# Performance work log

Measured on AMD Instinct MI355X. Metric: run time of the kernel, lower is better.

The kernel has to match this reference:

```python
import jax, jax.numpy as jnp
import numpy as np

T = 100      # sequence length / output times
B = 2048     # batch
DT = 0.02    # euler step == spacing of ts -> one step per interval
CLAMP = 6.0
LOG2PI = float(np.log(2.0 * np.pi))
sp = jax.nn.softplus


def setup_inputs() -> dict:
    key = jax.random.key(0)
    ks = jax.random.split(key, 20)
    rn = lambda k, s, sc=1.0: jax.random.normal(k, s, dtype=jnp.float32) * sc
    inp = {}
    inp['xs'] = rn(ks[0], (T, B, 3, 50))
    inp['ts'] = jnp.arange(T, dtype=jnp.float32) * DT
    inp['eps0'] = rn(ks[1], (B, 6))
    inp['dW'] = rn(ks[2], (T - 1, B, 6)) * np.sqrt(DT)  # Brownian increments ~ N(0, dt)
    # encoder: 150->30->30->15
    inp['eW1'] = rn(ks[3], (150, 30), 150 ** -0.5); inp['eb1'] = jnp.zeros((30,), jnp.float32)
    inp['eW2'] = rn(ks[4], (30, 30), 30 ** -0.5);   inp['eb2'] = jnp.zeros((30,), jnp.float32)
    inp['eW3'] = rn(ks[5], (30, 15), 30 ** -0.5);   inp['eb3'] = jnp.zeros((15,), jnp.float32)
    # decoder: 6->30->30->100
    inp['dcW1'] = rn(ks[6], (6, 30), 6 ** -0.5);    inp['dcb1'] = jnp.zeros((30,), jnp.float32)
    inp['dcW2'] = rn(ks[7], (30, 30), 30 ** -0.5);  inp['dcb2'] = jnp.zeros((30,), jnp.float32)
    inp['dcW3'] = rn(ks[8], (30, 100), 30 ** -0.5); inp['dcb3'] = jnp.zeros((100,), jnp.float32)
    # f_net: (6+1+3)=10 -> 30 -> 6
    inp['fW1'] = rn(ks[9], (10, 30), 10 ** -0.5);   inp['fb1'] = jnp.zeros((30,), jnp.float32)
    inp['fW2'] = rn(ks[10], (30, 6), 30 ** -0.5);   inp['fb2'] = jnp.zeros((6,), jnp.float32)
    # h_net: (6+1)=7 -> 30 -> 6
    inp['hW1'] = rn(ks[11], (7, 30), 7 ** -0.5);    inp['hb1'] = jnp.zeros((30,), jnp.float32)
    inp['hW2'] = rn(ks[12], (30, 6), 30 ** -0.5);   inp['hb2'] = jnp.zeros((6,), jnp.float32)
    # 6 g_nets stacked: 2 -> 30 -> 1 (sigmoid)
    inp['gW1'] = rn(ks[13], (6, 2, 30), 2 ** -0.5); inp['gb1'] = jnp.zeros((6, 30), jnp.float32)
    inp['gW2'] = rn(ks[14], (6, 30, 1), 30 ** -0.5); inp['gb2'] = jnp.zeros((6, 1), jnp.float32)
    inp['pz0_mean'] = jnp.zeros((1, 6), jnp.float32)
    inp['pz0_logstd'] = jnp.zeros((1, 6), jnp.float32)
    return inp


def _forward(xs, ts, eps0, dW, eW1, eb1, eW2, eb2, eW3, eb3,
             dcW1, dcb1, dcW2, dcb2, dcW3, dcb3,
             fW1, fb1, fW2, fb2, hW1, hb1, hW2, hb2,
             gW1, gb1, gW2, gb2, pz0_mean, pz0_logstd):
    # ---- encoder on time-reversed xs ----
    xse = jnp.flip(xs, 0).reshape(T, B, 150)
    e = sp(xse @ eW1 + eb1)
    e = sp(e @ eW2 + eb2)
    e = e @ eW3 + eb3                         # [T,B,15]
    qz0_mean = e[-1, :, :6]
    qz0_logstd = e[-1, :, 6:12]
    ctx = jnp.flip(e[..., 12:15], 0)           # [T,B,3]

    z0 = qz0_mean + jnp.exp(jnp.clip(qz0_logstd, -CLAMP, CLAMP)) * eps0

    # ---- Euler-Maruyama with logqp (one step per ts interval) ----
    def step(z, sc):
        k, dWk = sc
        t = ts[k]
        dtk = ts[k + 1] - ts[k]
        c = ctx[jnp.minimum(k + 1, T - 1)]     # searchsorted(ts, t, right=True) clamped
        tb = jnp.broadcast_to(t, (B, 1)).astype(z.dtype)
        f = sp(jnp.concatenate([tb, z, c], 1) @ fW1 + fb1) @ fW2 + fb2
        h = sp(jnp.concatenate([tb, z], 1) @ hW1 + hb1) @ hW2 + hb2
        gin = jnp.stack([jnp.broadcast_to(t, (B, 6)).astype(z.dtype), z], -1)  # [B,6,2]
        gh = sp(jnp.einsum('bdi,dih->bdh', gin, gW1) + gb1)
        g = jax.nn.sigmoid(jnp.einsum('bdh,dho->bdo', gh, gW2) + gb2)[..., 0]  # [B,6]
        u = (f - h) / g
        logr = 0.5 * jnp.sum(u * u, axis=1) * dtk   # [B]
        zn = z + f * dtk + g * dWk
        return zn, (zn, logr)

    _, (zs_tail, log_ratio) = jax.lax.scan(step, z0, (jnp.arange(T - 1), dW))
    zs = jnp.concatenate([z0[None], zs_tail], 0)   # [T,B,6]

    # ---- decoder + likelihood ----
    d = sp(zs @ dcW1 + dcb1)
    d = sp(d @ dcW2 + dcb2)
    d = d @ dcW3 + dcb3                        # [T,B,100]
    xm, xl = d[..., :50], d[..., 50:]
    xsig = jnp.exp(jnp.clip(xl, -CLAMP, CLAMP))
    tgt = xs[:, :, -1, :]
    lp = -0.5 * ((tgt - xm) / xsig) ** 2 - jnp.log(xsig) - 0.5 * LOG2PI
    log_pxs = jnp.mean(jnp.sum(lp, axis=(0, 2)))

    # ---- KL(q(z0)||p(z0)) + path term ----
    sq = jnp.exp(jnp.clip(qz0_logstd, -CLAMP, CLAMP))
    spz = jnp.exp(jnp.clip(pz0_logstd, -CLAMP, CLAMP))
    kl = jnp.log(spz / sq) + (sq ** 2 + (qz0_mean - pz0_mean) ** 2) / (2.0 * spz ** 2) - 0.5
    logqp0 = jnp.mean(jnp.sum(kl, axis=1))
    logqp_path = jnp.mean(jnp.sum(log_ratio, axis=0))
    return log_pxs, logqp0 + logqp_path


def reference(xs, ts, eps0, dW, eW1, eb1, eW2, eb2, eW3, eb3,
              dcW1, dcb1, dcW2, dcb2, dcW3, dcb3,
              fW1, fb1, fW2, fb2, hW1, hb1, hW2, hb2,
              gW1, gb1, gW2, gb2, pz0_mean, pz0_logstd):
    return _forward(xs, ts, eps0, dW, eW1, eb1, eW2, eb2, eW3, eb3,
                    dcW1, dcb1, dcW2, dcb2, dcW3, dcb3,
                    fW1, fb1, fW2, fb2, hW1, hb1, hW2, hb2,
                    gW1, gb1, gW2, gb2, pz0_mean, pz0_logstd)
```

## Files before the change

### kernel.cpp

```cpp
#include <hip/hip_runtime.h>
#include <hip/hip_bf16.h>
#include <math.h>

#define Tn 100
#define Bn 2048

typedef int v2i __attribute__((ext_vector_type(2)));
typedef _Float16 h2v __attribute__((ext_vector_type(2)));

__device__ __forceinline__ float sp_f(float x) {
    float e = __expf(-fabsf(x));
    return fmaxf(x, 0.f) + __logf(1.f + e);
}
__device__ __forceinline__ float clamp6(float x) {
    return fminf(fmaxf(x, -6.f), 6.f);
}
__device__ __forceinline__ unsigned int packh2(float a, float b) {
    h2v h; h.x = (_Float16)a; h.y = (_Float16)b;
    return __builtin_bit_cast(unsigned int, h);
}
__device__ __forceinline__ float dot2f(unsigned int a, unsigned int b, float c) {
#if __has_builtin(__builtin_amdgcn_fdot2)
    return __builtin_amdgcn_fdot2(__builtin_bit_cast(h2v, a),
                                  __builtin_bit_cast(h2v, b), c, false);
#else
    h2v ha = __builtin_bit_cast(h2v, a), hb = __builtin_bit_cast(h2v, b);
    return fmaf((float)ha.y, (float)hb.y, fmaf((float)ha.x, (float)hb.x, c));
#endif
}

__device__ __forceinline__ float dpp_xor1(float x) {
    return __int_as_float(__builtin_amdgcn_mov_dpp(__float_as_int(x), 0xB1, 0xF, 0xF, 1));
}
__device__ __forceinline__ float dpp_xor2(float x) {
    return __int_as_float(__builtin_amdgcn_mov_dpp(__float_as_int(x), 0x4E, 0xF, 0xF, 1));
}
__device__ __forceinline__ float dpp_hmirror(float x) {
    return __int_as_float(__builtin_amdgcn_mov_dpp(__float_as_int(x), 0x141, 0xF, 0xF, 1));
}
__device__ __forceinline__ float dpp_ror8(float x) {
    return __int_as_float(__builtin_amdgcn_mov_dpp(__float_as_int(x), 0x128, 0xF, 0xF, 1));
}
template <int OFF>
__device__ __forceinline__ float swz(float x) {
    return __int_as_float(__builtin_amdgcn_ds_swizzle(__float_as_int(x), OFF));
}
__device__ __forceinline__ float xor16_sum(float x) {
#if __has_builtin(__builtin_amdgcn_permlane16_swap)
    v2i r = __builtin_amdgcn_permlane16_swap(__float_as_int(x), __float_as_int(x), false, false);
    return __int_as_float(r[0]) + __int_as_float(r[1]);
#else
    return x + swz<0x401F>(x);
#endif
}
__device__ __forceinline__ float other_half(float x) {
#if __has_builtin(__builtin_amdgcn_permlane32_swap)
    v2i r = __builtin_amdgcn_permlane32_swap(__float_as_int(x), __float_as_int(x), false, false);
    return (__int_as_float(r[0]) + __int_as_float(r[1])) - x;
#else
    return __shfl_xor(x, 32);
#endif
}

__device__ __forceinline__ void rowd2(float* ha, float* hb, const unsigned int* wrow,
                                      unsigned int xa, unsigned int xb) {
#pragma unroll
    for (int q = 0; q < 7; ++q) {
        uint4 wv = *(const uint4*)(wrow + 4 * q);
        ha[4 * q + 0] = dot2f(xa, wv.x, ha[4 * q + 0]);
        hb[4 * q + 0] = dot2f(xb, wv.x, hb[4 * q + 0]);
        ha[4 * q + 1] = dot2f(xa, wv.y, ha[4 * q + 1]);
        hb[4 * q + 1] = dot2f(xb, wv.y, hb[4 * q + 1]);
        ha[4 * q + 2] = dot2f(xa, wv.z, ha[4 * q + 2]);
        hb[4 * q + 2] = dot2f(xb, wv.z, hb[4 * q + 2]);
        ha[4 * q + 3] = dot2f(xa, wv.w, ha[4 * q + 3]);
        hb[4 * q + 3] = dot2f(xb, wv.w, hb[4 * q + 3]);
    }
    uint2 wt = *(const uint2*)(wrow + 28);
    ha[28] = dot2f(xa, wt.x, ha[28]);
    hb[28] = dot2f(xb, wt.x, hb[28]);
    ha[29] = dot2f(xa, wt.y, ha[29]);
    hb[29] = dot2f(xb, wt.y, hb[29]);
}
__device__ __forceinline__ void dot30_2(const float* ha, const float* hb,
                                        const float* wrow, float& ra, float& rb) {
    float a0 = 0.f, a1 = 0.f, b0 = 0.f, b1 = 0.f;
#pragma unroll
    for (int q = 0; q < 7; ++q) {
        float4 wv = *(const float4*)(wrow + 4 * q);
        a0 = fmaf(ha[4 * q + 0], wv.x, a0);
        b0 = fmaf(hb[4 * q + 0], wv.x, b0);
        a1 = fmaf(ha[4 * q + 1], wv.y, a1);
        b1 = fmaf(hb[4 * q + 1], wv.y, b1);
        a0 = fmaf(ha[4 * q + 2], wv.z, a0);
        b0 = fmaf(hb[4 * q + 2], wv.z, b0);
        a1 = fmaf(ha[4 * q + 3], wv.w, a1);
        b1 = fmaf(hb[4 * q + 3], wv.w, b1);
    }
    float2 wt = *(const float2*)(wrow + 28);
    a0 = fmaf(ha[28], wt.x, a0);
    b0 = fmaf(hb[28], wt.x, b0);
    a1 = fmaf(ha[29], wt.y, a1);
    b1 = fmaf(hb[29], wt.y, b1);
    ra = a0 + a1; rb = b0 + b1;
}
__device__ __forceinline__ void dot16p_2(const unsigned int* pa, const unsigned int* pb,
                                         const unsigned int* wrow, float& ra, float& rb) {
    float a0 = 0.f, a1 = 0.f, b0 = 0.f, b1 = 0.f;
#pragma unroll
    for (int q = 0; q < 4; ++q) {
        uint4 wv = *(const uint4*)(wrow + 4 * q);
        a0 = dot2f(pa[4 * q + 0], wv.x, a0);
        b0 = dot2f(pb[4 * q + 0], wv.x, b0);
        a1 = dot2f(pa[4 * q + 1], wv.y, a1);
        b1 = dot2f(pb[4 * q + 1], wv.y, b1);
        a0 = dot2f(pa[4 * q + 2], wv.z, a0);
        b0 = dot2f(pb[4 * q + 2], wv.z, b0);
        a1 = dot2f(pa[4 * q + 3], wv.w, a1);
        b1 = dot2f(pb[4 * q + 3], wv.w, b1);
    }
    ra = a0 + a1; rb = b0 + b1;
}

#define ENC_LOAD2(b0, b1, base)                                               \
    _Pragma("unroll")                                                         \
    for (int i = 0; i < 5; ++i) {                                             \
        b0[i] = *(const float2*)(x0 + (base) + 2 * i);                        \
        b1[i] = *(const float2*)(x1 + (base) + 2 * i);                        \
    }
#define ENC_COMP2(b0, b1, pb)                                                 \
    _Pragma("unroll")                                                         \
    for (int i = 0; i < 5; ++i) {                                             \
        unsigned int xa = packh2(b0[i].x, b0[i].y);                           \
        unsigned int xb = packh2(b1[i].x, b1[i].y);                           \
        rowd2(h1a, h1b, &wh1[((pb) + i) * 32], xa, xb);                       \
    }

__global__ __launch_bounds__(256) void enc_kernel(
    const float* __restrict__ xs,
    const float* __restrict__ eW1, const float* __restrict__ eb1,
    const float* __restrict__ eW2, const float* __restrict__ eb2,
    const float* __restrict__ eW3, const float* __restrict__ eb3,
    float* __restrict__ ctx, float* __restrict__ qm, float* __restrict__ qs)
{
    __shared__ __align__(16) unsigned int wh1[75 * 32];
    __shared__ __align__(16) unsigned int wh2[15 * 32];
    __shared__ __align__(16) float wf[555];

    for (int i = threadIdx.x; i < 75 * 30; i += 256) {
        int p = i / 30, j = i % 30;
        wh1[p * 32 + j] = packh2(eW1[(2 * p) * 30 + j], eW1[(2 * p + 1) * 30 + j]);
    }
    for (int i = threadIdx.x; i < 15 * 30; i += 256) {
        int p = i / 30, j = i % 30;
        wh2[p * 32 + j] = packh2(eW2[(2 * p) * 30 + j], eW2[(2 * p + 1) * 30 + j]);
    }
    if (threadIdx.x < 30) wf[threadIdx.x] = eb1[threadIdx.x];
    if (threadIdx.x >= 32 && threadIdx.x < 62) wf[30 + threadIdx.x - 32] = eb2[threadIdx.x - 32];
    for (int i = threadIdx.x; i < 90; i += 256) {
        int o = i / 30, j2 = i % 30;
        wf[60 + o * 32 + j2] = eW3[j2 * 15 + 12 + o];
    }
    for (int i = threadIdx.x; i < 360; i += 256) {
        int o = i / 30, j2 = i % 30;
        wf[156 + o * 32 + j2] = eW3[j2 * 15 + o];
    }
    if (threadIdx.x >= 64 && threadIdx.x < 79) wf[540 + threadIdx.x - 64] = eb3[threadIdx.x - 64];
    __syncthreads();

    int t = threadIdx.x;
    size_t base = (size_t)blockIdx.x * 512;
    size_t s0 = base + t, s1 = base + t + 256;
    const float* x0 = xs + s0 * 150;
    const float* x1 = xs + s1 * 150;

    float h1a[30], h1b[30];
#pragma unroll
    for (int j = 0; j < 30; ++j) { h1a[j] = wf[j]; h1b[j] = h1a[j]; }

    float2 A0[5], A1[5], B0[5], B1[5];
    ENC_LOAD2(A0, A1, 0)
    ENC_LOAD2(B0, B1, 10)
    int fb = 0;
#pragma unroll 1
    for (int it = 0; it < 6; ++it) {
        ENC_COMP2(A0, A1, fb / 2)
        ENC_LOAD2(A0, A1, fb + 20)
        ENC_COMP2(B0, B1, fb / 2 + 5)
        ENC_LOAD2(B0, B1, fb + 30)
        fb += 20;
    }
    ENC_COMP2(A0, A1, 60)
    ENC_LOAD2(A0, A1, 140)
    ENC_COMP2(B0, B1, 65)
    ENC_COMP2(A0, A1, 70)

#pragma unroll
    for (int j = 0; j < 30; ++j) { h1a[j] = sp_f(h1a[j]); h1b[j] = sp_f(h1b[j]); }

    unsigned int p1a[15], p1b[15];
#pragma unroll
    for (int p = 0; p < 15; ++p) {
        p1a[p] = packh2(h1a[2 * p], h1a[2 * p + 1]);
        p1b[p] = packh2(h1b[2 * p], h1b[2 * p + 1]);
    }
    float h2a[30], h2b[30];
#pragma unroll
    for (int j = 0; j < 30; ++j) { h2a[j] = wf[30 + j]; h2b[j] = h2a[j]; }
#pragma unroll
    for (int p = 0; p < 15; ++p)
        rowd2(h2a, h2b, &wh2[p * 32], p1a[p], p1b[p]);
#pragma unroll
    for (int j = 0; j < 30; ++j) { h2a[j] = sp_f(h2a[j]); h2b[j] = sp_f(h2b[j]); }

    float oa3[3], ob3[3];
#pragma unroll
    for (int o = 0; o < 3; ++o) {
        float ra, rb;
        dot30_2(h2a, h2b, &wf[60 + o * 32], ra, rb);
        oa3[o] = wf[540 + 12 + o] + ra;
        ob3[o] = wf[540 + 12 + o] + rb;
    }
    float* cp0 = ctx + s0 * 3;
    cp0[0] = oa3[0]; cp0[1] = oa3[1]; cp0[2] = oa3[2];
    float* cp1 = ctx + s1 * 3;
    cp1[0] = ob3[0]; cp1[1] = ob3[1]; cp1[2] = ob3[2];

    if (blockIdx.x < 4) {
#pragma unroll
        for (int o = 0; o < 12; ++o) {
            float ra, rb;
            dot30_2(h2a, h2b, &wf[156 + o * 32], ra, rb);
            float va = wf[540 + o] + ra, vb = wf[540 + o] + rb;
            if (o < 6) { qm[s0 * 6 + o] = va; qm[s1 * 6 + o] = vb; }
            else       { qs[s0 * 6 + o - 6] = va; qs[s1 * 6 + o - 6] = vb; }
        }
    }
}

__global__ __launch_bounds__(128, 4) void scan_kernel(
    const float* __restrict__ ts, const float* __restrict__ dWall,
    const float* __restrict__ fW1, const float* __restrict__ fb1,
    const float* __restrict__ fW2, const float* __restrict__ fb2,
    const float* __restrict__ hW1, const float* __restrict__ hb1,
    const float* __restrict__ hW2, const float* __restrict__ hb2,
    const float* __restrict__ gW1, const float* __restrict__ gb1,
    const float* __restrict__ gW2, const float* __restrict__ gb2,
    const float* __restrict__ ctx,
    const float* __restrict__ qm, const float* __restrict__ qs,
    const float* __restrict__ eps0, const float* __restrict__ pm,
    const float* __restrict__ ps,
    float* __restrict__ zsb, float* __restrict__ acc)
{
    int tid = threadIdx.x;
    int lane = tid & 63;
    int b = blockIdx.x;
    bool isA = tid < 64;

    __shared__ float sRec[99 * 12];
    __shared__ float exF[2][12];
    __shared__ float exG[2][8];

    for (int i = tid; i < 99 * 3; i += 128) {
        int k = i / 3, e = i % 3;
        float2 v = *(const float2*)(dWall + ((size_t)k * Bn + b) * 6 + e * 2);
        *(float2*)&sRec[k * 12 + e * 2] = v;
    }
    for (int i = tid; i < 99 * 3; i += 128) {
        int k = i / 3, e = i % 3;
        sRec[k * 12 + 6 + e] = ctx[((size_t)(k + 1) * Bn + b) * 3 + e];
    }
    for (int i = tid; i < 99; i += 128) {
        float t0 = ts[i], t1 = ts[i + 1];
        sRec[i * 12 + 9]  = 0.f;
        sRec[i * 12 + 10] = t0;
        sRec[i * 12 + 11] = t1 - t0;
    }

    float z[6];
    float zq = 0.f;
    float wl1[10], b1w, wl2[6], fb2v[6], hb2v[6];
    float gwa[4], gwb[4], gw2v[4], gbb[4], gb2v = 0.f, wselq = 0.f;
    int dL = 0;

    if (isA) {
        bool lower = lane < 32;
        int j = lane & 31;
        int jc = (j < 30) ? j : 29;
        bool jvalid = (j < 30);
#pragma unroll
        for (int i = 0; i < 10; ++i)
            wl1[i] = lower ? fW1[i * 30 + jc] : (i < 7 ? hW1[i * 30 + jc] : 0.f);
        b1w = lower ? fb1[jc] : hb1[jc];
#pragma unroll
        for (int d = 0; d < 6; ++d)
            wl2[d] = jvalid ? (lower ? fW2[jc * 6 + d] : hW2[jc * 6 + d]) : 0.f;
#pragma unroll
        for (int d = 0; d < 6; ++d) { fb2v[d] = fb2[d]; hb2v[d] = hb2[d]; }
#pragma unroll
        for (int d = 0; d < 6; ++d) {
            float m = qm[b * 6 + d];
            float sq = __expf(clamp6(qs[b * 6 + d]));
            z[d] = fmaf(sq, eps0[b * 6 + d], m);
        }
        if (tid == 0) {
            float* zp = zsb + (size_t)b * 6;
            *(float2*)(zp)     = make_float2(z[0], z[1]);
            *(float2*)(zp + 2) = make_float2(z[2], z[3]);
            *(float2*)(zp + 4) = make_float2(z[4], z[5]);
        }
    } else {
        int dL8 = lane >> 3;
        dL = (dL8 < 6) ? dL8 : 0;
        wselq = (dL8 < 6) ? 0.0625f : 0.f;
        int s = lane & 7;
#pragma unroll
        for (int u = 0; u < 4; ++u) {
            int jj = s + 8 * u;
            bool ok = (dL8 < 6) && (jj < 30);
            gwa[u]  = ok ? gW1[dL * 60 + jj] : 0.f;
            gwb[u]  = ok ? gW1[dL * 60 + 30 + jj] : 0.f;
            gw2v[u] = ok ? gW2[dL * 30 + jj] : 0.f;
            gbb[u]  = ok ? gb1[dL * 30 + jj] : 0.f;
        }
        gb2v = gb2[dL];
        {
            float m = qm[b * 6 + dL];
            float sq = __expf(clamp6(qs[b * 6 + dL]));
            zq = fmaf(sq, eps0[b * 6 + dL], m);
        }
        if (tid == 64) {
            float klsum = 0.f;
#pragma unroll
            for (int d = 0; d < 6; ++d) {
                float m = qm[b * 6 + d];
                float sq = __expf(clamp6(qs[b * 6 + d]));
                float spz = __expf(clamp6(ps[d]));
                float dm = m - pm[d];
                klsum += __logf(spz / sq) + (sq * sq + dm * dm) / (2.f * spz * spz) - 0.5f;
            }
            atomicAdd(&acc[1], klsum);
        }
    }

    __syncthreads();

    float pacc = 0.f;

    for (int k = 0; k < Tn - 1; ++k) {
        int kb = k & 1;

        if (isA) {
            float4 r0 = *(float4*)&sRec[k * 12];
            float4 r1 = *(float4*)&sRec[k * 12 + 4];
            float4 r2 = *(float4*)&sRec[k * 12 + 8];
            float t = r2.z, dt = r2.w;

            float a = fmaf(t, wl1[0], b1w);
#pragma unroll
            for (int i = 0; i < 6; ++i) a = fmaf(z[i], wl1[1 + i], a);
            a = fmaf(r1.z, wl1[7], a);
            a = fmaf(r1.w, wl1[8], a);
            a = fmaf(r2.x, wl1[9], a);
            float hid = sp_f(a);

            float pp[6];
#pragma unroll
            for (int d = 0; d < 6; ++d) pp[d] = hid * wl2[d];
#pragma unroll
            for (int d = 0; d < 6; ++d) pp[d] += dpp_xor1(pp[d]);
#pragma unroll
            for (int d = 0; d < 6; ++d) pp[d] += dpp_xor2(pp[d]);
#pragma unroll
            for (int d = 0; d < 6; ++d) pp[d] += dpp_hmirror(pp[d]);
#pragma unroll
            for (int d = 0; d < 6; ++d) pp[d] += dpp_ror8(pp[d]);
#pragma unroll
            for (int d = 0; d < 6; ++d) pp[d] = xor16_sum(pp[d]);
            float fvv[6], dfh[6];
            bool lower = lane < 32;
#pragma unroll
            for (int d = 0; d < 6; ++d) {
                float oth = other_half(pp[d]);
                float fsum = lower ? pp[d] : oth;
                float hsum = lower ? oth : pp[d];
                fvv[d] = fsum + fb2v[d];
                dfh[d] = fvv[d] - (hsum + hb2v[d]);
            }
            if (lane == 0) {
                *(float4*)&exF[kb][0] = make_float4(fvv[0], fvv[1], fvv[2], fvv[3]);
                *(float4*)&exF[kb][4] = make_float4(fvv[4], fvv[5], dfh[0], dfh[1]);
                *(float4*)&exF[kb][8] = make_float4(dfh[2], dfh[3], dfh[4], dfh[5]);
            }

            __syncthreads();

            float4 g03 = *(float4*)&exG[kb][0];
            float2 g45 = *(float2*)&exG[kb][4];
            float gl[6] = { g03.x, g03.y, g03.z, g03.w, g45.x, g45.y };
            float dwv[6] = { r0.x, r0.y, r0.z, r0.w, r1.x, r1.y };
#pragma unroll
            for (int d = 0; d < 6; ++d)
                z[d] = fmaf(gl[d], dwv[d], fmaf(fvv[d], dt, z[d]));

            if (tid == 0) {
                float* zp = zsb + ((size_t)(k + 1) * Bn + b) * 6;
                *(float2*)(zp)     = make_float2(z[0], z[1]);
                *(float2*)(zp + 2) = make_float2(z[2], z[3]);
                *(float2*)(zp + 4) = make_float2(z[4], z[5]);
            }
        } else {
            float2 tdt = *(float2*)&sRec[k * 12 + 10];
            float t = tdt.x, dt = tdt.y;
            float dwq = sRec[k * 12 + dL];

            float ga = 0.f;
#pragma unroll
            for (int u = 0; u < 4; ++u) {
                float pre = fmaf(t, gwa[u], gbb[u]);
                pre = fmaf(zq, gwb[u], pre);
                ga = fmaf(sp_f(pre), gw2v[u], ga);
            }
            ga += dpp_xor1(ga);
            ga += dpp_xor2(ga);
            ga += dpp_hmirror(ga);
            float gacc = ga + gb2v;
            float e = __expf(-gacc);
            float rg = 1.f + e;
            float gval = __builtin_amdgcn_rcpf(rg);
            if ((lane & 7) == 0 && (lane >> 3) < 6)
                exG[kb][dL] = gval;

            __syncthreads();

            float fq  = exF[kb][dL];
            float dfq = exF[kb][6 + dL];
            float u = dfq * rg;
            pacc = fmaf(wselq * dt, u * u, pacc);
            zq = fmaf(gval, dwq, fmaf(fq, dt, zq));
        }
    }
    if (!isA) {
#pragma unroll
        for (int mm = 1; mm <= 32; mm <<= 1) pacc += __shfl_xor(pacc, mm);
        if (tid == 64) atomicAdd(&acc[2], pacc);
    }
}

#define DEC_TLOAD(b0, b1, base)                                               \
    _Pragma("unroll")                                                         \
    for (int i = 0; i < 5; ++i) {                                             \
        b0[i] = *(const float2*)(tg0 + (base) + 2 * i);                       \
        b1[i] = *(const float2*)(tg1 + (base) + 2 * i);                       \
    }
#define DEC_LCOMP(b0, b1, base)                                               \
    _Pragma("unroll")                                                         \
    for (int i = 0; i < 10; ++i) {                                            \
        int ff = (base) + i;                                                  \
        float dma, dmb, dla, dlb;                                             \
        dot16p_2(p2a, p2b, &wh3[ff * 16], dma, dmb);                          \
        dot16p_2(p2a, p2b, &wh3[(50 + ff) * 16], dla, dlb);                   \
        float xma = wd[256 + ff] + dma, xmb = wd[256 + ff] + dmb;             \
        float cla = clamp6(wd[256 + 50 + ff] + dla);                          \
        float clb = clamp6(wd[256 + 50 + ff] + dlb);                          \
        float tva = (i & 1) ? b0[i >> 1].y : b0[i >> 1].x;                    \
        float tvb = (i & 1) ? b1[i >> 1].y : b1[i >> 1].x;                    \
        float ua = (tva - xma) * __expf(-cla);                                \
        float ub = (tvb - xmb) * __expf(-clb);                                \
        lpa += -0.5f * ua * ua - cla - 0.91893853320467274f;                  \
        lpb += -0.5f * ub * ub - clb - 0.91893853320467274f;                  \
    }

__global__ __launch_bounds__(256) void dec_kernel(
    const float* __restrict__ zsb, const float* __restrict__ xs,
    const float* __restrict__ dcW1, const float* __restrict__ dcb1,
    const float* __restrict__ dcW2, const float* __restrict__ dcb2,
    const float* __restrict__ dcW3, const float* __restrict__ dcb3,
    float* __restrict__ acc)
{
    __shared__ __align__(16) float wd[356];
    __shared__ __align__(16) unsigned int wh2d[15 * 32];
    __shared__ __align__(16) unsigned int wh3[100 * 16];

    for (int i = threadIdx.x; i < 180; i += 256) wd[(i / 30) * 32 + (i % 30)] = dcW1[i];
    if (threadIdx.x < 30) wd[192 + threadIdx.x] = dcb1[threadIdx.x];
    if (threadIdx.x >= 32 && threadIdx.x < 62) wd[224 + threadIdx.x - 32] = dcb2[threadIdx.x - 32];
    for (int i = threadIdx.x; i < 100; i += 256) wd[256 + i] = dcb3[i];
    for (int i = threadIdx.x; i < 15 * 30; i += 256) {
        int p = i / 30, j = i % 30;
        wh2d[p * 32 + j] = packh2(dcW2[(2 * p) * 30 + j], dcW2[(2 * p + 1) * 30 + j]);
    }
    for (int i = threadIdx.x; i < 100 * 16; i += 256) {
        int ff = i / 16, p = i % 16;
        wh3[i] = (p < 15) ? packh2(dcW3[(2 * p) * 100 + ff], dcW3[(2 * p + 1) * 100 + ff]) : 0u;
    }
    __syncthreads();

    int t = threadIdx.x;
    size_t base = (size_t)blockIdx.x * 512;
    size_t s0 = base + t, s1 = base + t + 256;

    float za[6], zb[6];
    {
        const float* zp0 = zsb + s0 * 6;
        const float* zp1 = zsb + s1 * 6;
#pragma unroll
        for (int i = 0; i < 3; ++i) {
            float2 v0 = *(const float2*)(zp0 + 2 * i);
            float2 v1 = *(const float2*)(zp1 + 2 * i);
            za[2 * i] = v0.x; za[2 * i + 1] = v0.y;
            zb[2 * i] = v1.x; zb[2 * i + 1] = v1.y;
        }
    }

    float h1a[30], h1b[30];
#pragma unroll
    for (int j = 0; j < 30; ++j) { h1a[j] = wd[192 + j]; h1b[j] = h1a[j]; }
#pragma unroll
    for (int i = 0; i < 6; ++i) {
        float via = za[i], vib = zb[i];
        const float* wrow = &wd[i * 32];
#pragma unroll
        for (int q = 0; q < 7; ++q) {
            float4 wv = *(const float4*)(wrow + 4 * q);
            h1a[4 * q + 0] = fmaf(via, wv.x, h1a[4 * q + 0]);
            h1b[4 * q + 0] = fmaf(vib, wv.x, h1b[4 * q + 0]);
            h1a[4 * q + 1] = fmaf(via, wv.y, h1a[4 * q + 1]);
            h1b[4 * q + 1] = fmaf(vib, wv.y, h1b[4 * q + 1]);
            h1a[4 * q + 2] = fmaf(via, wv.z, h1a[4 * q + 2]);
            h1b[4 * q + 2] = fmaf(vib, wv.z, h1b[4 * q + 2]);
            h1a[4 * q + 3] = fmaf(via, wv.w, h1a[4 * q + 3]);
            h1b[4 * q + 3] = fmaf(vib, wv.w, h1b[4 * q + 3]);
        }
        float2 wt = *(const float2*)(wrow + 28);
        h1a[28] = fmaf(via, wt.x, h1a[28]);
        h1b[28] = fmaf(vib, wt.x, h1b[28]);
        h1a[29] = fmaf(via, wt.y, h1a[29]);
        h1b[29] = fmaf(vib, wt.y, h1b[29]);
    }
#pragma unroll
    for (int j = 0; j < 30; ++j) { h1a[j] = sp_f(h1a[j]); h1b[j] = sp_f(h1b[j]); }

    unsigned int p1a[15], p1b[15];
#pragma unroll
    for (int p = 0; p < 15; ++p) {
        p1a[p] = packh2(h1a[2 * p], h1a[2 * p + 1]);
        p1b[p] = packh2(h1b[2 * p], h1b[2 * p + 1]);
    }
    float h2a[30], h2b[30];
#pragma unroll
    for (int j = 0; j < 30; ++j) { h2a[j] = wd[224 + j]; h2b[j] = h2a[j]; }
#pragma unroll
    for (int p = 0; p < 15; ++p)
        rowd2(h2a, h2b, &wh2d[p * 32], p1a[p], p1b[p]);
#pragma unroll
    for (int j = 0; j < 30; ++j) { h2a[j] = sp_f(h2a[j]); h2b[j] = sp_f(h2b[j]); }

    unsigned int p2a[16], p2b[16];
#pragma unroll
    for (int p = 0; p < 15; ++p) {
        p2a[p] = packh2(h2a[2 * p], h2a[2 * p + 1]);
        p2b[p] = packh2(h2b[2 * p], h2b[2 * p + 1]);
    }
    p2a[15] = 0u; p2b[15] = 0u;

    const float* tg0 = xs + s0 * 150 + 100;
    const float* tg1 = xs + s1 * 150 + 100;
    float lpa = 0.f, lpb = 0.f;
    float2 TA0[5], TA1[5], TB0[5], TB1[5];
    DEC_TLOAD(TA0, TA1, 0)
    DEC_TLOAD(TB0, TB1, 10)
    DEC_LCOMP(TA0, TA1, 0)
    DEC_TLOAD(TA0, TA1, 20)
    DEC_LCOMP(TB0, TB1, 10)
    DEC_TLOAD(TB0, TB1, 30)
    DEC_LCOMP(TA0, TA1, 20)
    DEC_TLOAD(TA0, TA1, 40)
    DEC_LCOMP(TB0, TB1, 30)
    DEC_LCOMP(TA0, TA1, 40)

    float lpacc = lpa + lpb;
#pragma unroll
    for (int mm = 1; mm <= 32; mm <<= 1) lpacc += __shfl_xor(lpacc, mm);
    __shared__ float red[4];
    if ((threadIdx.x & 63) == 0) red[threadIdx.x >> 6] = lpacc;
    __syncthreads();
    if (threadIdx.x == 0) atomicAdd(&acc[0], red[0] + red[1] + red[2] + red[3]);
}

__global__ void final_kernel(const float* __restrict__ acc, float* __restrict__ out)
{
    out[0] = acc[0] * (1.f / (float)Bn);
    out[1] = (acc[1] + acc[2]) * (1.f / (float)Bn);
}

extern "C" void kernel_launch(void* const* d_in, const int* in_sizes, int n_in,
                              void* d_out, int out_size, void* d_ws, size_t ws_size,
                              hipStream_t stream)
{
    const float* xs   = (const float*)d_in[0];
    const float* ts   = (const float*)d_in[1];
    const float* eps0 = (const float*)d_in[2];
    const float* dW   = (const float*)d_in[3];
    const float* eW1  = (const float*)d_in[4];
    const float* eb1  = (const float*)d_in[5];
    const float* eW2  = (const float*)d_in[6];
    const float* eb2  = (const float*)d_in[7];
    const float* eW3  = (const float*)d_in[8];
    const float* eb3  = (const float*)d_in[9];
    const float* dcW1 = (const float*)d_in[10];
    const float* dcb1 = (const float*)d_in[11];
    const float* dcW2 = (const float*)d_in[12];
    const float* dcb2 = (const float*)d_in[13];
    const float* dcW3 = (const float*)d_in[14];
    const float* dcb3 = (const float*)d_in[15];
    const float* fW1  = (const float*)d_in[16];
    const float* fb1  = (const float*)d_in[17];
    const float* fW2  = (const float*)d_in[18];
    const float* fb2  = (const float*)d_in[19];
    const float* hW1  = (const float*)d_in[20];
    const float* hb1  = (const float*)d_in[21];
    const float* hW2  = (const float*)d_in[22];
    const float* hb2  = (const float*)d_in[23];
    const float* gW1  = (const float*)d_in[24];
    const float* gb1  = (const float*)d_in[25];
    const float* gW2  = (const float*)d_in[26];
    const float* gb2  = (const float*)d_in[27];
    const float* pm   = (const float*)d_in[28];
    const float* ps   = (const float*)d_in[29];

    float* ws  = (float*)d_ws;
    float* acc = ws;
    float* ctx = ws + 16;
    float* qm  = ctx + 614400;
    float* qs  = qm + 12288;
    float* zs  = qs + 12288;
    float* out = (float*)d_out;

    hipMemsetAsync(acc, 0, 16 * sizeof(float), stream);
    enc_kernel<<<400, 256, 0, stream>>>(xs, eW1, eb1, eW2, eb2, eW3, eb3, ctx, qm, qs);
    scan_kernel<<<2048, 128, 0, stream>>>(ts, dW, fW1, fb1, fW2, fb2, hW1, hb1,
                                          hW2, hb2, gW1, gb1, gW2, gb2, ctx,
                                          qm, qs, eps0, pm, ps, zs, acc);
    dec_kernel<<<400, 256, 0, stream>>>(zs, xs, dcW1, dcb1, dcW2, dcb2, dcW3, dcb3, acc);
    final_kernel<<<1, 1, 0, stream>>>(acc, out);
}
```

Measured before the change: 244.0 us.

## Shrink enc/dec blocks to one wave, buffer z history in LDS, prefetch scan records

The encoder and decoder now run as 64-thread blocks over four times as many blocks. This spreads the 400-block grid across more CUs, at the cost of each block re-staging its weights into LDS. In the scan kernel, the per-step global z writes go to a shared-memory history that is flushed with coalesced stores at the end. The next step's sRec records are prefetched before the barrier, and the first-layer dot product is split into two accumulation chains to shorten the serial dependency. The decoder's cross-wave shared reduction is replaced by a direct atomic per wave.

```diff
diff --git a/kernel.cpp b/kernel.cpp
--- a/kernel.cpp
+++ b/kernel.cpp
@@ -136,7 +136,7 @@
         rowd2(h1a, h1b, &wh1[((pb) + i) * 32], xa, xb);                       \
     }
 
-__global__ __launch_bounds__(256) void enc_kernel(
+__global__ __launch_bounds__(64) void enc_kernel(
     const float* __restrict__ xs,
     const float* __restrict__ eW1, const float* __restrict__ eb1,
     const float* __restrict__ eW2, const float* __restrict__ eb2,
@@ -147,30 +147,29 @@
     __shared__ __align__(16) unsigned int wh2[15 * 32];
     __shared__ __align__(16) float wf[555];
 
-    for (int i = threadIdx.x; i < 75 * 30; i += 256) {
+    int tid = threadIdx.x;
+    for (int i = tid; i < 75 * 30; i += 64) {
         int p = i / 30, j = i % 30;
         wh1[p * 32 + j] = packh2(eW1[(2 * p) * 30 + j], eW1[(2 * p + 1) * 30 + j]);
     }
-    for (int i = threadIdx.x; i < 15 * 30; i += 256) {
+    for (int i = tid; i < 15 * 30; i += 64) {
         int p = i / 30, j = i % 30;
         wh2[p * 32 + j] = packh2(eW2[(2 * p) * 30 + j], eW2[(2 * p + 1) * 30 + j]);
     }
-    if (threadIdx.x < 30) wf[threadIdx.x] = eb1[threadIdx.x];
-    if (threadIdx.x >= 32 && threadIdx.x < 62) wf[30 + threadIdx.x - 32] = eb2[threadIdx.x - 32];
-    for (int i = threadIdx.x; i < 90; i += 256) {
+    if (tid < 30) { wf[tid] = eb1[tid]; wf[30 + tid] = eb2[tid]; }
+    for (int i = tid; i < 90; i += 64) {
         int o = i / 30, j2 = i % 30;
         wf[60 + o * 32 + j2] = eW3[j2 * 15 + 12 + o];
     }
-    for (int i = threadIdx.x; i < 360; i += 256) {
+    for (int i = tid; i < 360; i += 64) {
         int o = i / 30, j2 = i % 30;
         wf[156 + o * 32 + j2] = eW3[j2 * 15 + o];
     }
-    if (threadIdx.x >= 64 && threadIdx.x < 79) wf[540 + threadIdx.x - 64] = eb3[threadIdx.x - 64];
+    if (tid < 15) wf[540 + tid] = eb3[tid];
     __syncthreads();
 
-    int t = threadIdx.x;
-    size_t base = (size_t)blockIdx.x * 512;
-    size_t s0 = base + t, s1 = base + t + 256;
+    size_t base = (size_t)blockIdx.x * 128;
+    size_t s0 = base + tid, s1 = base + tid + 64;
     const float* x0 = xs + s0 * 150;
     const float* x1 = xs + s1 * 150;
 
@@ -226,7 +225,7 @@
     float* cp1 = ctx + s1 * 3;
     cp1[0] = ob3[0]; cp1[1] = ob3[1]; cp1[2] = ob3[2];
 
-    if (blockIdx.x < 4) {
+    if (blockIdx.x < 16) {
 #pragma unroll
         for (int o = 0; o < 12; ++o) {
             float ra, rb;
@@ -260,6 +259,7 @@
     __shared__ float sRec[99 * 12];
     __shared__ float exF[2][12];
     __shared__ float exG[2][8];
+    __shared__ float zhist[100 * 6];
 
     for (int i = tid; i < 99 * 3; i += 128) {
         int k = i / 3, e = i % 3;
@@ -303,11 +303,9 @@
             float sq = __expf(clamp6(qs[b * 6 + d]));
             z[d] = fmaf(sq, eps0[b * 6 + d], m);
         }
-        if (tid == 0) {
-            float* zp = zsb + (size_t)b * 6;
-            *(float2*)(zp)     = make_float2(z[0], z[1]);
-            *(float2*)(zp + 2) = make_float2(z[2], z[3]);
-            *(float2*)(zp + 4) = make_float2(z[4], z[5]);
+        if (lane == 0) {
+#pragma unroll
+            for (int d = 0; d < 6; ++d) zhist[d] = z[d];
         }
     } else {
         int dL8 = lane >> 3;
@@ -347,22 +345,36 @@
 
     float pacc = 0.f;
 
+    float4 r0, r1, r2;
+    float2 tdt;
+    float dwq = 0.f;
+    if (isA) {
+        r0 = *(float4*)&sRec[0];
+        r1 = *(float4*)&sRec[4];
+        r2 = *(float4*)&sRec[8];
+    } else {
+        tdt = *(float2*)&sRec[10];
+        dwq = sRec[dL];
+    }
+
     for (int k = 0; k < Tn - 1; ++k) {
         int kb = k & 1;
+        int kn = (k < Tn - 2) ? (k + 1) * 12 : k * 12;
 
         if (isA) {
-            float4 r0 = *(float4*)&sRec[k * 12];
-            float4 r1 = *(float4*)&sRec[k * 12 + 4];
-            float4 r2 = *(float4*)&sRec[k * 12 + 8];
             float t = r2.z, dt = r2.w;
 
-            float a = fmaf(t, wl1[0], b1w);
-#pragma unroll
-            for (int i = 0; i < 6; ++i) a = fmaf(z[i], wl1[1 + i], a);
-            a = fmaf(r1.z, wl1[7], a);
-            a = fmaf(r1.w, wl1[8], a);
-            a = fmaf(r2.x, wl1[9], a);
-            float hid = sp_f(a);
+            float a0 = fmaf(t, wl1[0], b1w);
+            a0 = fmaf(z[0], wl1[1], a0);
+            a0 = fmaf(z[1], wl1[2], a0);
+            a0 = fmaf(z[2], wl1[3], a0);
+            a0 = fmaf(z[3], wl1[4], a0);
+            float a1 = z[4] * wl1[5];
+            a1 = fmaf(z[5], wl1[6], a1);
+            a1 = fmaf(r1.z, wl1[7], a1);
+            a1 = fmaf(r1.w, wl1[8], a1);
+            a1 = fmaf(r2.x, wl1[9], a1);
+            float hid = sp_f(a0 + a1);
 
             float pp[6];
 #pragma unroll
@@ -392,6 +404,9 @@
                 *(float4*)&exF[kb][4] = make_float4(fvv[4], fvv[5], dfh[0], dfh[1]);
                 *(float4*)&exF[kb][8] = make_float4(dfh[2], dfh[3], dfh[4], dfh[5]);
             }
+            float4 n0 = *(float4*)&sRec[kn];
+            float4 n1 = *(float4*)&sRec[kn + 4];
+            float4 n2 = *(float4*)&sRec[kn + 8];
 
             __syncthreads();
 
@@ -403,16 +418,14 @@
             for (int d = 0; d < 6; ++d)
                 z[d] = fmaf(gl[d], dwv[d], fmaf(fvv[d], dt, z[d]));
 
-            if (tid == 0) {
-                float* zp = zsb + ((size_t)(k + 1) * Bn + b) * 6;
-                *(float2*)(zp)     = make_float2(z[0], z[1]);
-                *(float2*)(zp + 2) = make_float2(z[2], z[3]);
-                *(float2*)(zp + 4) = make_float2(z[4], z[5]);
+            if (lane == 0) {
+                float* zp = &zhist[(k + 1) * 6];
+#pragma unroll
+                for (int d = 0; d < 6; ++d) zp[d] = z[d];
             }
+            r0 = n0; r1 = n1; r2 = n2;
         } else {
-            float2 tdt = *(float2*)&sRec[k * 12 + 10];
             float t = tdt.x, dt = tdt.y;
-            float dwq = sRec[k * 12 + dL];
 
             float ga = 0.f;
 #pragma unroll
@@ -431,6 +444,9 @@
             if ((lane & 7) == 0 && (lane >> 3) < 6)
                 exG[kb][dL] = gval;
 
+            float2 ntdt = *(float2*)&sRec[kn + 10];
+            float ndwq = sRec[kn + dL];
+
             __syncthreads();
 
             float fq  = exF[kb][dL];
@@ -438,12 +454,19 @@
             float u = dfq * rg;
             pacc = fmaf(wselq * dt, u * u, pacc);
             zq = fmaf(gval, dwq, fmaf(fq, dt, zq));
+            tdt = ntdt; dwq = ndwq;
         }
     }
     if (!isA) {
 #pragma unroll
         for (int mm = 1; mm <= 32; mm <<= 1) pacc += __shfl_xor(pacc, mm);
         if (tid == 64) atomicAdd(&acc[2], pacc);
+    }
+
+    __syncthreads();
+    for (int i = tid; i < 300; i += 128) {
+        int k = i / 3, p = i % 3;
+        *(float2*)&zsb[((size_t)k * Bn + b) * 6 + 2 * p] = *(float2*)&zhist[k * 6 + 2 * p];
     }
 }
 
@@ -471,7 +494,7 @@
         lpb += -0.5f * ub * ub - clb - 0.91893853320467274f;                  \
     }
 
-__global__ __launch_bounds__(256) void dec_kernel(
+__global__ __launch_bounds__(64) void dec_kernel(
     const float* __restrict__ zsb, const float* __restrict__ xs,
     const float* __restrict__ dcW1, const float* __restrict__ dcb1,
     const float* __restrict__ dcW2, const float* __restrict__ dcb2,
@@ -482,23 +505,22 @@
     __shared__ __align__(16) unsigned int wh2d[15 * 32];
     __shared__ __align__(16) unsigned int wh3[100 * 16];
 
-    for (int i = threadIdx.x; i < 180; i += 256) wd[(i / 30) * 32 + (i % 30)] = dcW1[i];
-    if (threadIdx.x < 30) wd[192 + threadIdx.x] = dcb1[threadIdx.x];
-    if (threadIdx.x >= 32 && threadIdx.x < 62) wd[224 + threadIdx.x - 32] = dcb2[threadIdx.x - 32];
-    for (int i = threadIdx.x; i < 100; i += 256) wd[256 + i] = dcb3[i];
-    for (int i = threadIdx.x; i < 15 * 30; i += 256) {
+    int tid = threadIdx.x;
+    for (int i = tid; i < 180; i += 64) wd[(i / 30) * 32 + (i % 30)] = dcW1[i];
+    if (tid < 30) { wd[192 + tid] = dcb1[tid]; wd[224 + tid] = dcb2[tid]; }
+    for (int i = tid; i < 100; i += 64) wd[256 + i] = dcb3[i];
+    for (int i = tid; i < 15 * 30; i += 64) {
         int p = i / 30, j = i % 30;
         wh2d[p * 32 + j] = packh2(dcW2[(2 * p) * 30 + j], dcW2[(2 * p + 1) * 30 + j]);
     }
-    for (int i = threadIdx.x; i < 100 * 16; i += 256) {
+    for (int i = tid; i < 100 * 16; i += 64) {
         int ff = i / 16, p = i % 16;
         wh3[i] = (p < 15) ? packh2(dcW3[(2 * p) * 100 + ff], dcW3[(2 * p + 1) * 100 + ff]) : 0u;
     }
     __syncthreads();
 
-    int t = threadIdx.x;
-    size_t base = (size_t)blockIdx.x * 512;
-    size_t s0 = base + t, s1 = base + t + 256;
+    size_t base = (size_t)blockIdx.x * 128;
+    size_t s0 = base + tid, s1 = base + tid + 64;
 
     float za[6], zb[6];
     {
@@ -582,10 +604,7 @@
     float lpacc = lpa + lpb;
 #pragma unroll
     for (int mm = 1; mm <= 32; mm <<= 1) lpacc += __shfl_xor(lpacc, mm);
-    __shared__ float red[4];
-    if ((threadIdx.x & 63) == 0) red[threadIdx.x >> 6] = lpacc;
-    __syncthreads();
-    if (threadIdx.x == 0) atomicAdd(&acc[0], red[0] + red[1] + red[2] + red[3]);
+    if (tid == 0) atomicAdd(&acc[0], lpacc);
 }
 
 __global__ void final_kernel(const float* __restrict__ acc, float* __restrict__ out)
@@ -638,10 +657,10 @@
     float* out = (float*)d_out;
 
     hipMemsetAsync(acc, 0, 16 * sizeof(float), stream);
-    enc_kernel<<<400, 256, 0, stream>>>(xs, eW1, eb1, eW2, eb2, eW3, eb3, ctx, qm, qs);
+    enc_kernel<<<1600, 64, 0, stream>>>(xs, eW1, eb1, eW2, eb2, eW3, eb3, ctx, qm, qs);
     scan_kernel<<<2048, 128, 0, stream>>>(ts, dW, fW1, fb1, fW2, fb2, hW1, hb1,
                                           hW2, hb2, gW1, gb1, gW2, gb2, ctx,
                                           qm, qs, eps0, pm, ps, zs, acc);
-    dec_kernel<<<400, 256, 0, stream>>>(zs, xs, dcW1, dcb1, dcW2, dcb2, dcW3, dcb3, acc);
+    dec_kernel<<<1600, 64, 0, stream>>>(zs, xs, dcW1, dcb1, dcW2, dcb2, dcW3, dcb3, acc);
     final_kernel<<<1, 1, 0, stream>>>(acc, out);
 }
```

New measurement: 287.3 us. 1.18x slower.
